# Kernel optimization log

Measured on AMD Instinct MI355X. Metric: run time of the kernel, lower is better.

Reference implementation:

```python
import jax, jax.numpy as jnp
import numpy as np

A, B = 0.0, 1.0
U_LEFT, U_RIGHT = 0.0, 0.0
BOUNDARY_PENALTY = 10.0
N_POINTS = 32768
K_TEST = 1024  # sine test functions
LAYERS = [1, 256, 256, 256, 1]


def setup_inputs() -> dict:
    key = jax.random.key(0)
    ks = jax.random.split(key, 2 + len(LAYERS) - 1)
    # Gauss-Lobatto-like nodes: sorted points in (A, B)
    x = jnp.sort(jax.random.uniform(ks[0], (N_POINTS, 1), dtype=jnp.float32,
                                    minval=A, maxval=B), axis=0)
    # positive quadrature weights, scaled so sum(weights) ~ (B - A)
    weights = jax.random.uniform(ks[1], (N_POINTS,), dtype=jnp.float32) * (2.0 * (B - A) / N_POINTS)
    inp = {"x": x, "weights": weights}
    for i in range(len(LAYERS) - 1):
        fin, fout = LAYERS[i], LAYERS[i + 1]
        inp[f"W{i}"] = jax.random.normal(ks[2 + i], (fin, fout), dtype=jnp.float32) / np.sqrt(fin).astype(np.float32)
        inp[f"b{i}"] = jnp.zeros((fout,), dtype=jnp.float32)
    return inp


def _mlp(h, params):
    # tanh MLP, no activation on the last layer (matches MLP.forward)
    n = len(params)
    for i, (W, b) in enumerate(params):
        h = h @ W + b
        if i < n - 1:
            h = jnp.tanh(h)
    return h


def reference(x, weights, W0, b0, W1, b1, W2, b2, W3, b3):
    params = [(W0, b0), (W1, b1), (W2, b2), (W3, b3)]
    xf = x[:, 0]                                   # [N]

    u = _mlp(x, params)                            # [N, 1]

    # u_xx at every quadrature node via grad-of-grad, vmapped over points
    def u_scalar(xv):
        return _mlp(xv.reshape(1, 1), params)[0, 0]
    u_xx = jax.vmap(jax.grad(jax.grad(u_scalar)))(xf)   # [N]

    # analytic sine test functions v_k(x) = sin(pi k x), k = 1..K
    k = jnp.arange(1, K_TEST + 1, dtype=x.dtype)        # [K]
    test = jnp.sin(jnp.pi * k[:, None] * xf[None, :])   # [K, N]

    source = jnp.sin(jnp.pi * xf)                       # f(x) on the grid, [N]

    # batched quadrature: one matvec replaces the per-k Integrate loop
    Fk = test @ (weights * source)                      # [K]
    Rk = -(test @ (weights * u_xx))                     # [K]  (method 1: -int u_xx v_k)

    loss_interior = jnp.mean((Rk - Fk) ** 2)
    loss_boundary = 0.5 * BOUNDARY_PENALTY * (
        (u[0, 0] - U_LEFT) ** 2 + (u[-1, 0] - U_RIGHT) ** 2
    )
    return jnp.stack([loss_interior, loss_boundary])
```

## Files before the change

### kernel.cpp

```cpp
#include <hip/hip_runtime.h>
#include <cmath>

#define N_PTS 32768
#define HID   256
#define KTEST 1024
#define MB    32
#define RS    264
#define SKC   256
#define SKYB  (N_PTS / SKC)
#define SKGRID (4 * SKYB)
#define NBLK  (N_PTS / MB)

typedef float  f32x4  __attribute__((ext_vector_type(4)));
typedef short  s16x4  __attribute__((ext_vector_type(4)));
typedef short  s16x8  __attribute__((ext_vector_type(8)));
typedef __bf16 bf16x8 __attribute__((ext_vector_type(8)));

__device__ __forceinline__ float b2f(unsigned short s) {
    return __uint_as_float(((unsigned int)s) << 16);
}
__device__ __forceinline__ unsigned short cvt16(float x) {
    return __builtin_bit_cast(unsigned short, (__bf16)x);
}
__device__ __forceinline__ void split2(float x, unsigned short& hi, unsigned short& lo) {
    unsigned int b = __float_as_uint(x);
    hi = (unsigned short)(b >> 16);
    float hf = __uint_as_float(b & 0xFFFF0000u);
    lo = cvt16(x - hf);
}
__device__ __forceinline__ float fast_tanh(float z) {
    float e = __expf(2.0f * z);
    return 1.0f - 2.0f / (e + 1.0f);
}

__global__ __launch_bounds__(64) void wswz_kernel(
    const float* __restrict__ W1, const float* __restrict__ W2,
    unsigned short* __restrict__ Wh1, unsigned short* __restrict__ Wl1,
    unsigned short* __restrict__ Wh2, unsigned short* __restrict__ Wl2,
    unsigned int* __restrict__ counter)
{
    const int lane = threadIdx.x;
    const int t  = blockIdx.x;
    const int kc = blockIdx.y;
    const float* W = blockIdx.z ? W2 : W1;
    unsigned short* Wh = blockIdx.z ? Wh2 : Wh1;
    unsigned short* Wl = blockIdx.z ? Wl2 : Wl1;
    const int q = lane >> 4, ln = lane & 15;
    const int n = t * 16 + ln;
    const int kbase = kc * 32 + q * 8;

    s16x8 hv, lv;
    #pragma unroll
    for (int j = 0; j < 8; ++j) {
        unsigned short h, l;
        split2(W[(kbase + j) * HID + n], h, l);
        hv[j] = (short)h; lv[j] = (short)l;
    }
    const int out = ((t * 8 + kc) * 64 + lane) * 8;
    *(s16x8*)(Wh + out) = hv;
    *(s16x8*)(Wl + out) = lv;

    if (lane == 0 && t == 0 && kc == 0 && blockIdx.z == 0)
        *counter = 0u;
}

__global__ __launch_bounds__(512, 4) void mlp_kernel(
    const float* __restrict__ x, const float* __restrict__ wq,
    const float* __restrict__ W0, const float* __restrict__ b0,
    const float* __restrict__ b1v, const float* __restrict__ b2v,
    const float* __restrict__ W3, const float* __restrict__ b3,
    const unsigned short* __restrict__ W1h, const unsigned short* __restrict__ W1l,
    const unsigned short* __restrict__ W2h, const unsigned short* __restrict__ W2l,
    float* __restrict__ u_arr, float* __restrict__ d_arr,
    float* __restrict__ partF)
{
    __shared__ __align__(16) unsigned short Hb[3][MB][RS];
    __shared__ float sx_h[MB], sx_l[MB], sd[MB];

    const int tid = threadIdx.x;
    const int gp0 = blockIdx.x * MB;

    {
        const int m = tid & 31, seg = tid >> 5;
        const float xm = x[gp0 + m];
        #pragma unroll
        for (int jb = 0; jb < 4; ++jb) {
            s16x4 vy, vyp, vypp;
            #pragma unroll
            for (int jl = 0; jl < 4; ++jl) {
                const int j = seg * 16 + jb * 4 + jl;
                float w = W0[j];
                float z = fmaf(xm, w, b0[j]);
                float y = fast_tanh(z);
                float s = 1.0f - y * y;
                float yp = s * w;
                float ypp = -2.0f * y * yp * w;
                vy[jl]   = (short)cvt16(y);
                vyp[jl]  = (short)cvt16(yp);
                vypp[jl] = (short)cvt16(ypp);
            }
            const int j0 = seg * 16 + jb * 4;
            *(s16x4*)&Hb[0][m][j0] = vy;
            *(s16x4*)&Hb[1][m][j0] = vyp;
            *(s16x4*)&Hb[2][m][j0] = vypp;
        }
    }
    __syncthreads();

    const int lane = tid & 63, wv = tid >> 6;
    const int q = lane >> 4, ln = lane & 15;

    const int fragbase = (wv * 2) * 8 * 512 + lane * 8;

    for (int layer = 0; layer < 2; ++layer) {
        const unsigned short* __restrict__ WhW = (layer ? W2h : W1h) + fragbase;
        const unsigned short* __restrict__ WlW = (layer ? W2l : W1l) + fragbase;
        const float* __restrict__ bb = layer ? b2v : b1v;

        f32x4 acc[3][2][2];
        #pragma unroll
        for (int s = 0; s < 3; ++s)
            #pragma unroll
            for (int mf = 0; mf < 2; ++mf)
                #pragma unroll
                for (int nt = 0; nt < 2; ++nt)
                    acc[s][mf][nt] = (f32x4){0.f, 0.f, 0.f, 0.f};

        s16x8 bh[2][2], bl[2][2];
        #pragma unroll
        for (int nt = 0; nt < 2; ++nt) {
            bh[0][nt] = *(const s16x8*)(WhW + nt * 4096);
            bl[0][nt] = *(const s16x8*)(WlW + nt * 4096);
        }

        int cur = 0;
        for (int kc = 0; kc < 8; ++kc) {
            const int nxt = cur ^ 1;
            if (kc < 7) {
                #pragma unroll
                for (int nt = 0; nt < 2; ++nt) {
                    const int off = nt * 4096 + (kc + 1) * 512;
                    bh[nxt][nt] = *(const s16x8*)(WhW + off);
                    bl[nxt][nt] = *(const s16x8*)(WlW + off);
                }
            }
            s16x8 av[3][2];
            #pragma unroll
            for (int s = 0; s < 3; ++s)
                #pragma unroll
                for (int mf = 0; mf < 2; ++mf)
                    av[s][mf] = *(const s16x8*)&Hb[s][mf * 16 + ln][kc * 32 + q * 8];
            #pragma unroll
            for (int s = 0; s < 3; ++s)
                #pragma unroll
                for (int mf = 0; mf < 2; ++mf)
                    #pragma unroll
                    for (int nt = 0; nt < 2; ++nt) {
                        acc[s][mf][nt] = __builtin_amdgcn_mfma_f32_16x16x32_bf16(
                            __builtin_bit_cast(bf16x8, av[s][mf]),
                            __builtin_bit_cast(bf16x8, bh[cur][nt]), acc[s][mf][nt], 0, 0, 0);
                        acc[s][mf][nt] = __builtin_amdgcn_mfma_f32_16x16x32_bf16(
                            __builtin_bit_cast(bf16x8, av[s][mf]),
                            __builtin_bit_cast(bf16x8, bl[cur][nt]), acc[s][mf][nt], 0, 0, 0);
                    }
            cur = nxt;
        }
        __syncthreads();

        #pragma unroll
        for (int nt = 0; nt < 2; ++nt) {
            const int c = wv * 32 + nt * 16 + ln;
            const float bias = bb[c];
            #pragma unroll
            for (int mf = 0; mf < 2; ++mf) {
                #pragma unroll
                for (int i = 0; i < 4; ++i) {
                    const int r = mf * 16 + q * 4 + i;
                    float z   = acc[0][mf][nt][i] + bias;
                    float zp  = acc[1][mf][nt][i];
                    float zpp = acc[2][mf][nt][i];
                    float y  = fast_tanh(z);
                    float s  = 1.0f - y * y;
                    float yp = s * zp;
                    float ypp = fmaf(s, zpp, -2.0f * y * yp * zp);
                    Hb[0][r][c] = cvt16(y);
                    if (layer == 0) Hb[1][r][c] = cvt16(yp);
                    Hb[2][r][c] = cvt16(ypp);
                }
            }
        }
        __syncthreads();
    }

    float* psum = (float*)&Hb[1][0][0];
    {
        const int m = tid & 31, seg = tid >> 5;
        float su = 0.f, sx = 0.f;
        #pragma unroll
        for (int jj8 = 0; jj8 < 2; ++jj8) {
            const int j0 = seg * 16 + jj8 * 8;
            s16x8 vy = *(const s16x8*)&Hb[0][m][j0];
            s16x8 vx = *(const s16x8*)&Hb[2][m][j0];
            #pragma unroll
            for (int u = 0; u < 8; ++u) {
                float w3 = W3[j0 + u];
                su = fmaf(b2f((unsigned short)vy[u]), w3, su);
                sx = fmaf(b2f((unsigned short)vx[u]), w3, sx);
            }
        }
        psum[(0 * 16 + seg) * 32 + m] = su;
        psum[(1 * 16 + seg) * 32 + m] = sx;
    }
    __syncthreads();
    if (tid < MB) {
        float u = b3[0], uxx = 0.f;
        #pragma unroll
        for (int s2 = 0; s2 < 16; ++s2) {
            u   += psum[s2 * 32 + tid];
            uxx += psum[(16 + s2) * 32 + tid];
        }
        const int gp = gp0 + tid;
        u_arr[gp] = u;
        float xv = x[gp];
        float dv = -wq[gp] * (uxx + sinpif(xv));
        d_arr[gp] = dv;
        float xh = __uint_as_float(__float_as_uint(xv) & 0xFFFFF000u);
        sx_h[tid] = xh * 0.5f;
        sx_l[tid] = (xv - xh) * 0.5f;
        sd[tid]   = dv;
    }

    if (partF) {
        __syncthreads();
        const float k1 = (float)(tid + 1);
        const float k2 = (float)(tid + 513);
        float s1 = 0.f, s2 = 0.f;
        #pragma unroll 8
        for (int i = 0; i < MB; ++i) {
            float xh = sx_h[i], xl = sx_l[i], dv = sd[i];
            float f1 = __builtin_amdgcn_fractf(k1 * xh);
            float t1 = __builtin_amdgcn_fractf(fmaf(k1, xl, f1));
            s1 = fmaf(__builtin_amdgcn_sinf(t1), dv, s1);
            float f2 = __builtin_amdgcn_fractf(k2 * xh);
            float t2 = __builtin_amdgcn_fractf(fmaf(k2, xl, f2));
            s2 = fmaf(__builtin_amdgcn_sinf(t2), dv, s2);
        }
        partF[blockIdx.x * KTEST + tid]       = s1;
        partF[blockIdx.x * KTEST + tid + 512] = s2;
    }
}

__global__ __launch_bounds__(256) void reduce_kernel(
    const float* __restrict__ part, const float* __restrict__ u_arr,
    unsigned int* __restrict__ counter, float* __restrict__ red_g,
    float* __restrict__ out)
{
    __shared__ float sm[8][33];
    __shared__ int lastFlag;

    const int tid = threadIdx.x;
    const int kk = tid & 31;
    const int ch = tid >> 5;
    const int k = blockIdx.x * 32 + kk;

    const float* P = part + (ch << 7) * KTEST + k;
    float s = 0.f;
    #pragma unroll 8
    for (int b = 0; b < 128; ++b) s += P[b << 10];
    sm[ch][kk] = s;
    __syncthreads();

    if (tid < 32) {
        float t = 0.f;
        #pragma unroll
        for (int j = 0; j < 8; ++j) t += sm[j][kk];
        float sq = t * t;
        #pragma unroll
        for (int off = 16; off > 0; off >>= 1) sq += __shfl_down(sq, off, 64);
        if (kk == 0) red_g[blockIdx.x] = sq;
    }
    __threadfence();
    if (tid == 0)
        lastFlag = (atomicAdd(counter, 1u) == 31u);
    __syncthreads();
    if (!lastFlag) return;
    __threadfence();

    if (tid < 32) {
        float v = red_g[tid];
        #pragma unroll
        for (int off = 16; off > 0; off >>= 1) v += __shfl_down(v, off, 64);
        if (tid == 0) {
            out[0] = v * (1.0f / (float)KTEST);
            float u0 = u_arr[0], uN = u_arr[N_PTS - 1];
            out[1] = 5.0f * (u0 * u0 + uN * uN);
        }
    }
}

__global__ __launch_bounds__(256) void sk_loss_kernel(
    const float* __restrict__ x, const float* __restrict__ d_arr,
    const float* __restrict__ u_arr, float* __restrict__ part,
    unsigned int* __restrict__ counter, float* __restrict__ out)
{
    __shared__ float xs_h[SKC], xs_l[SKC], ds[SKC];
    __shared__ float red[4];
    __shared__ int lastFlag;

    const int tid = threadIdx.x;
    const int k = blockIdx.x * 256 + tid;
    const int i0 = blockIdx.y * SKC;

    {
        float xv = x[i0 + tid];
        float xh = __uint_as_float(__float_as_uint(xv) & 0xFFFFF000u);
        xs_h[tid] = xh * 0.5f;
        xs_l[tid] = (xv - xh) * 0.5f;
        ds[tid]   = d_arr[i0 + tid];
    }
    __syncthreads();

    const float kf = (float)(k + 1);
    float s = 0.f;
    #pragma unroll 8
    for (int i = 0; i < SKC; ++i) {
        float A = kf * xs_h[i];
        float f = __builtin_amdgcn_fractf(A);
        float t = __builtin_amdgcn_fractf(fmaf(kf, xs_l[i], f));
        s = fmaf(__builtin_amdgcn_sinf(t), ds[i], s);
    }
    part[blockIdx.y * KTEST + k] = s;

    __threadfence();
    if (tid == 0)
        lastFlag = (atomicAdd(counter, 1u) == (unsigned)(SKGRID - 1));
    __syncthreads();
    if (!lastFlag) return;
    __threadfence();

    float a0 = 0.f, a1 = 0.f, a2 = 0.f, a3 = 0.f;
    const float* P = part + tid * 4;
    for (int yb = 0; yb < SKYB; ++yb) {
        f32x4 v = *(const f32x4*)(P + yb * KTEST);
        a0 += v[0]; a1 += v[1]; a2 += v[2]; a3 += v[3];
    }
    float sq = a0 * a0 + a1 * a1 + a2 * a2 + a3 * a3;
    #pragma unroll
    for (int off = 32; off > 0; off >>= 1) sq += __shfl_down(sq, off, 64);
    if ((tid & 63) == 0) red[tid >> 6] = sq;
    __syncthreads();
    if (tid == 0) {
        float t = red[0] + red[1] + red[2] + red[3];
        out[0] = t * (1.0f / (float)KTEST);
        float u0 = u_arr[0], uN = u_arr[N_PTS - 1];
        out[1] = 5.0f * (u0 * u0 + uN * uN);
    }
}

extern "C" void kernel_launch(void* const* d_in, const int* in_sizes, int n_in,
                              void* d_out, int out_size, void* d_ws, size_t ws_size,
                              hipStream_t stream)
{
    const float* x  = (const float*)d_in[0];
    const float* wq = (const float*)d_in[1];
    const float* W0 = (const float*)d_in[2];
    const float* b0 = (const float*)d_in[3];
    const float* W1 = (const float*)d_in[4];
    const float* b1 = (const float*)d_in[5];
    const float* W2 = (const float*)d_in[6];
    const float* b2 = (const float*)d_in[7];
    const float* W3 = (const float*)d_in[8];
    const float* b3 = (const float*)d_in[9];
    float* out = (float*)d_out;

    float* ws    = (float*)d_ws;
    float* u_arr = ws;
    float* d_arr = ws + N_PTS;
    float* partS = ws + 2 * N_PTS;
    unsigned short* W1h = (unsigned short*)(ws + 2 * N_PTS + SKYB * KTEST);
    unsigned short* W1l = W1h + HID * HID;
    unsigned short* W2h = W1l + HID * HID;
    unsigned short* W2l = W2h + HID * HID;
    unsigned int* counter = (unsigned int*)(W2l + HID * HID);
    float* red_g = ws + 327696;
    float* partF = ws + 327744;
    const size_t need = (size_t)(327744 + NBLK * KTEST) * sizeof(float);
    const bool fused = ws_size >= need;

    wswz_kernel<<<dim3(16, 8, 2), 64, 0, stream>>>(W1, W2, W1h, W1l, W2h, W2l, counter);
    mlp_kernel<<<NBLK, 512, 0, stream>>>(x, wq, W0, b0, b1, b2, W3, b3,
                                         W1h, W1l, W2h, W2l, u_arr, d_arr,
                                         fused ? partF : nullptr);
    if (fused)
        reduce_kernel<<<32, 256, 0, stream>>>(partF, u_arr, counter, red_g, out);
    else
        sk_loss_kernel<<<dim3(4, SKYB), 256, 0, stream>>>(x, d_arr, u_arr, partS, counter, out);
}
```

Before: 131.4 us.

## Fuse sine-projection reduction into MLP kernel via sharded atomics and last-block finish

```diff
diff --git a/kernel.cpp b/kernel.cpp
--- a/kernel.cpp
+++ b/kernel.cpp
@@ -6,10 +6,8 @@
 #define KTEST 1024
 #define MB    32
 #define RS    264
-#define SKC   256
-#define SKYB  (N_PTS / SKC)
-#define SKGRID (4 * SKYB)
 #define NBLK  (N_PTS / MB)
+#define NSHADOW 8
 
 typedef float  f32x4  __attribute__((ext_vector_type(4)));
 typedef short  s16x4  __attribute__((ext_vector_type(4)));
@@ -37,7 +35,7 @@
     const float* __restrict__ W1, const float* __restrict__ W2,
     unsigned short* __restrict__ Wh1, unsigned short* __restrict__ Wl1,
     unsigned short* __restrict__ Wh2, unsigned short* __restrict__ Wl2,
-    unsigned int* __restrict__ counter)
+    unsigned int* __restrict__ counter, float* __restrict__ Rk8)
 {
     const int lane = threadIdx.x;
     const int t  = blockIdx.x;
@@ -60,8 +58,11 @@
     *(s16x8*)(Wh + out) = hv;
     *(s16x8*)(Wl + out) = lv;
 
-    if (lane == 0 && t == 0 && kc == 0 && blockIdx.z == 0)
-        *counter = 0u;
+    if (blockIdx.z == 0) {
+        const int idx = (blockIdx.y * 16 + blockIdx.x) * 64 + lane;
+        Rk8[idx] = 0.f;
+        if (idx == 0) *counter = 0u;
+    }
 }
 
 __global__ __launch_bounds__(512, 4) void mlp_kernel(
@@ -71,11 +72,13 @@
     const float* __restrict__ W3, const float* __restrict__ b3,
     const unsigned short* __restrict__ W1h, const unsigned short* __restrict__ W1l,
     const unsigned short* __restrict__ W2h, const unsigned short* __restrict__ W2l,
-    float* __restrict__ u_arr, float* __restrict__ d_arr,
-    float* __restrict__ partF)
+    float* __restrict__ u_arr, float* __restrict__ Rk8,
+    unsigned int* __restrict__ counter, float* __restrict__ out)
 {
     __shared__ __align__(16) unsigned short Hb[3][MB][RS];
     __shared__ float sx_h[MB], sx_l[MB], sd[MB];
+    __shared__ float red8[8];
+    __shared__ int lastFlag;
 
     const int tid = threadIdx.x;
     const int gp0 = blockIdx.x * MB;
@@ -121,16 +124,16 @@
         #pragma unroll
         for (int s = 0; s < 3; ++s)
             #pragma unroll
-            for (int mf = 0; mf < 2; ++mf)
-                #pragma unroll
-                for (int nt = 0; nt < 2; ++nt)
-                    acc[s][mf][nt] = (f32x4){0.f, 0.f, 0.f, 0.f};
+            for (int mt2 = 0; mt2 < 2; ++mt2)
+                #pragma unroll
+                for (int pt = 0; pt < 2; ++pt)
+                    acc[s][mt2][pt] = (f32x4){0.f, 0.f, 0.f, 0.f};
 
         s16x8 bh[2][2], bl[2][2];
         #pragma unroll
-        for (int nt = 0; nt < 2; ++nt) {
-            bh[0][nt] = *(const s16x8*)(WhW + nt * 4096);
-            bl[0][nt] = *(const s16x8*)(WlW + nt * 4096);
+        for (int mt2 = 0; mt2 < 2; ++mt2) {
+            bh[0][mt2] = *(const s16x8*)(WhW + mt2 * 4096);
+            bl[0][mt2] = *(const s16x8*)(WlW + mt2 * 4096);
         }
 
         int cur = 0;
@@ -138,55 +141,59 @@
             const int nxt = cur ^ 1;
             if (kc < 7) {
                 #pragma unroll
-                for (int nt = 0; nt < 2; ++nt) {
-                    const int off = nt * 4096 + (kc + 1) * 512;
-                    bh[nxt][nt] = *(const s16x8*)(WhW + off);
-                    bl[nxt][nt] = *(const s16x8*)(WlW + off);
+                for (int mt2 = 0; mt2 < 2; ++mt2) {
+                    const int off = mt2 * 4096 + (kc + 1) * 512;
+                    bh[nxt][mt2] = *(const s16x8*)(WhW + off);
+                    bl[nxt][mt2] = *(const s16x8*)(WlW + off);
                 }
             }
             s16x8 av[3][2];
             #pragma unroll
             for (int s = 0; s < 3; ++s)
                 #pragma unroll
-                for (int mf = 0; mf < 2; ++mf)
-                    av[s][mf] = *(const s16x8*)&Hb[s][mf * 16 + ln][kc * 32 + q * 8];
+                for (int pt = 0; pt < 2; ++pt)
+                    av[s][pt] = *(const s16x8*)&Hb[s][pt * 16 + ln][kc * 32 + q * 8];
             #pragma unroll
             for (int s = 0; s < 3; ++s)
                 #pragma unroll
-                for (int mf = 0; mf < 2; ++mf)
+                for (int mt2 = 0; mt2 < 2; ++mt2)
                     #pragma unroll
-                    for (int nt = 0; nt < 2; ++nt) {
-                        acc[s][mf][nt] = __builtin_amdgcn_mfma_f32_16x16x32_bf16(
-                            __builtin_bit_cast(bf16x8, av[s][mf]),
-                            __builtin_bit_cast(bf16x8, bh[cur][nt]), acc[s][mf][nt], 0, 0, 0);
-                        acc[s][mf][nt] = __builtin_amdgcn_mfma_f32_16x16x32_bf16(
-                            __builtin_bit_cast(bf16x8, av[s][mf]),
-                            __builtin_bit_cast(bf16x8, bl[cur][nt]), acc[s][mf][nt], 0, 0, 0);
+                    for (int pt = 0; pt < 2; ++pt) {
+                        acc[s][mt2][pt] = __builtin_amdgcn_mfma_f32_16x16x32_bf16(
+                            __builtin_bit_cast(bf16x8, bh[cur][mt2]),
+                            __builtin_bit_cast(bf16x8, av[s][pt]), acc[s][mt2][pt], 0, 0, 0);
+                        acc[s][mt2][pt] = __builtin_amdgcn_mfma_f32_16x16x32_bf16(
+                            __builtin_bit_cast(bf16x8, bl[cur][mt2]),
+                            __builtin_bit_cast(bf16x8, av[s][pt]), acc[s][mt2][pt], 0, 0, 0);
                     }
             cur = nxt;
         }
         __syncthreads();
 
         #pragma unroll
-        for (int nt = 0; nt < 2; ++nt) {
-            const int c = wv * 32 + nt * 16 + ln;
-            const float bias = bb[c];
-            #pragma unroll
-            for (int mf = 0; mf < 2; ++mf) {
+        for (int pt = 0; pt < 2; ++pt) {
+            const int p = pt * 16 + ln;
+            #pragma unroll
+            for (int mt2 = 0; mt2 < 2; ++mt2) {
+                const int cb = (wv * 2 + mt2) * 16 + q * 4;
+                const f32x4 b4 = *(const f32x4*)&bb[cb];
+                s16x4 vy, vyp, vypp;
                 #pragma unroll
                 for (int i = 0; i < 4; ++i) {
-                    const int r = mf * 16 + q * 4 + i;
-                    float z   = acc[0][mf][nt][i] + bias;
-                    float zp  = acc[1][mf][nt][i];
-                    float zpp = acc[2][mf][nt][i];
+                    float z   = acc[0][mt2][pt][i] + b4[i];
+                    float zp  = acc[1][mt2][pt][i];
+                    float zpp = acc[2][mt2][pt][i];
                     float y  = fast_tanh(z);
                     float s  = 1.0f - y * y;
                     float yp = s * zp;
                     float ypp = fmaf(s, zpp, -2.0f * y * yp * zp);
-                    Hb[0][r][c] = cvt16(y);
-                    if (layer == 0) Hb[1][r][c] = cvt16(yp);
-                    Hb[2][r][c] = cvt16(ypp);
+                    vy[i]   = (short)cvt16(y);
+                    vyp[i]  = (short)cvt16(yp);
+                    vypp[i] = (short)cvt16(ypp);
                 }
+                *(s16x4*)&Hb[0][p][cb] = vy;
+                if (layer == 0) *(s16x4*)&Hb[1][p][cb] = vyp;
+                *(s16x4*)&Hb[2][p][cb] = vypp;
             }
         }
         __syncthreads();
@@ -223,15 +230,14 @@
         u_arr[gp] = u;
         float xv = x[gp];
         float dv = -wq[gp] * (uxx + sinpif(xv));
-        d_arr[gp] = dv;
         float xh = __uint_as_float(__float_as_uint(xv) & 0xFFFFF000u);
         sx_h[tid] = xh * 0.5f;
         sx_l[tid] = (xv - xh) * 0.5f;
         sd[tid]   = dv;
     }
 
-    if (partF) {
-        __syncthreads();
+    __syncthreads();
+    {
         const float k1 = (float)(tid + 1);
         const float k2 = (float)(tid + 513);
         float s1 = 0.f, s2 = 0.f;
@@ -245,113 +251,34 @@
             float t2 = __builtin_amdgcn_fractf(fmaf(k2, xl, f2));
             s2 = fmaf(__builtin_amdgcn_sinf(t2), dv, s2);
         }
-        partF[blockIdx.x * KTEST + tid]       = s1;
-        partF[blockIdx.x * KTEST + tid + 512] = s2;
-    }
-}
-
-__global__ __launch_bounds__(256) void reduce_kernel(
-    const float* __restrict__ part, const float* __restrict__ u_arr,
-    unsigned int* __restrict__ counter, float* __restrict__ red_g,
-    float* __restrict__ out)
-{
-    __shared__ float sm[8][33];
-    __shared__ int lastFlag;
-
-    const int tid = threadIdx.x;
-    const int kk = tid & 31;
-    const int ch = tid >> 5;
-    const int k = blockIdx.x * 32 + kk;
-
-    const float* P = part + (ch << 7) * KTEST + k;
-    float s = 0.f;
-    #pragma unroll 8
-    for (int b = 0; b < 128; ++b) s += P[b << 10];
-    sm[ch][kk] = s;
-    __syncthreads();
-
-    if (tid < 32) {
-        float t = 0.f;
-        #pragma unroll
-        for (int j = 0; j < 8; ++j) t += sm[j][kk];
-        float sq = t * t;
-        #pragma unroll
-        for (int off = 16; off > 0; off >>= 1) sq += __shfl_down(sq, off, 64);
-        if (kk == 0) red_g[blockIdx.x] = sq;
-    }
+        float* myRk = Rk8 + (blockIdx.x & (NSHADOW - 1)) * KTEST;
+        atomicAdd(&myRk[tid], s1);
+        atomicAdd(&myRk[tid + 512], s2);
+    }
+
     __threadfence();
     if (tid == 0)
-        lastFlag = (atomicAdd(counter, 1u) == 31u);
+        lastFlag = (atomicAdd(counter, 1u) == (unsigned)(NBLK - 1));
     __syncthreads();
     if (!lastFlag) return;
     __threadfence();
 
-    if (tid < 32) {
-        float v = red_g[tid];
-        #pragma unroll
-        for (int off = 16; off > 0; off >>= 1) v += __shfl_down(v, off, 64);
-        if (tid == 0) {
-            out[0] = v * (1.0f / (float)KTEST);
-            float u0 = u_arr[0], uN = u_arr[N_PTS - 1];
-            out[1] = 5.0f * (u0 * u0 + uN * uN);
-        }
-    }
-}
-
-__global__ __launch_bounds__(256) void sk_loss_kernel(
-    const float* __restrict__ x, const float* __restrict__ d_arr,
-    const float* __restrict__ u_arr, float* __restrict__ part,
-    unsigned int* __restrict__ counter, float* __restrict__ out)
-{
-    __shared__ float xs_h[SKC], xs_l[SKC], ds[SKC];
-    __shared__ float red[4];
-    __shared__ int lastFlag;
-
-    const int tid = threadIdx.x;
-    const int k = blockIdx.x * 256 + tid;
-    const int i0 = blockIdx.y * SKC;
-
-    {
-        float xv = x[i0 + tid];
-        float xh = __uint_as_float(__float_as_uint(xv) & 0xFFFFF000u);
-        xs_h[tid] = xh * 0.5f;
-        xs_l[tid] = (xv - xh) * 0.5f;
-        ds[tid]   = d_arr[i0 + tid];
-    }
-    __syncthreads();
-
-    const float kf = (float)(k + 1);
-    float s = 0.f;
-    #pragma unroll 8
-    for (int i = 0; i < SKC; ++i) {
-        float A = kf * xs_h[i];
-        float f = __builtin_amdgcn_fractf(A);
-        float t = __builtin_amdgcn_fractf(fmaf(kf, xs_l[i], f));
-        s = fmaf(__builtin_amdgcn_sinf(t), ds[i], s);
-    }
-    part[blockIdx.y * KTEST + k] = s;
-
-    __threadfence();
-    if (tid == 0)
-        lastFlag = (atomicAdd(counter, 1u) == (unsigned)(SKGRID - 1));
-    __syncthreads();
-    if (!lastFlag) return;
-    __threadfence();
-
-    float a0 = 0.f, a1 = 0.f, a2 = 0.f, a3 = 0.f;
-    const float* P = part + tid * 4;
-    for (int yb = 0; yb < SKYB; ++yb) {
-        f32x4 v = *(const f32x4*)(P + yb * KTEST);
-        a0 += v[0]; a1 += v[1]; a2 += v[2]; a3 += v[3];
-    }
-    float sq = a0 * a0 + a1 * a1 + a2 * a2 + a3 * a3;
+    float t0 = 0.f, t1 = 0.f;
+    #pragma unroll
+    for (int j = 0; j < NSHADOW; ++j) {
+        t0 += Rk8[j * KTEST + tid];
+        t1 += Rk8[j * KTEST + tid + 512];
+    }
+    float sq = t0 * t0 + t1 * t1;
     #pragma unroll
     for (int off = 32; off > 0; off >>= 1) sq += __shfl_down(sq, off, 64);
-    if ((tid & 63) == 0) red[tid >> 6] = sq;
+    if ((tid & 63) == 0) red8[tid >> 6] = sq;
     __syncthreads();
     if (tid == 0) {
-        float t = red[0] + red[1] + red[2] + red[3];
-        out[0] = t * (1.0f / (float)KTEST);
+        float tt = 0.f;
+        #pragma unroll
+        for (int j = 0; j < 8; ++j) tt += red8[j];
+        out[0] = tt * (1.0f / (float)KTEST);
         float u0 = u_arr[0], uN = u_arr[N_PTS - 1];
         out[1] = 5.0f * (u0 * u0 + uN * uN);
     }
@@ -375,24 +302,16 @@
 
     float* ws    = (float*)d_ws;
     float* u_arr = ws;
-    float* d_arr = ws + N_PTS;
-    float* partS = ws + 2 * N_PTS;
-    unsigned short* W1h = (unsigned short*)(ws + 2 * N_PTS + SKYB * KTEST);
+    float* Rk8   = ws + N_PTS;
+    unsigned short* W1h = (unsigned short*)(ws + N_PTS + NSHADOW * KTEST);
     unsigned short* W1l = W1h + HID * HID;
     unsigned short* W2h = W1l + HID * HID;
     unsigned short* W2l = W2h + HID * HID;
     unsigned int* counter = (unsigned int*)(W2l + HID * HID);
-    float* red_g = ws + 327696;
-    float* partF = ws + 327744;
-    const size_t need = (size_t)(327744 + NBLK * KTEST) * sizeof(float);
-    const bool fused = ws_size >= need;
-
-    wswz_kernel<<<dim3(16, 8, 2), 64, 0, stream>>>(W1, W2, W1h, W1l, W2h, W2l, counter);
+
+    wswz_kernel<<<dim3(16, 8, 2), 64, 0, stream>>>(W1, W2, W1h, W1l, W2h, W2l,
+                                                   counter, Rk8);
     mlp_kernel<<<NBLK, 512, 0, stream>>>(x, wq, W0, b0, b1, b2, W3, b3,
-                                         W1h, W1l, W2h, W2l, u_arr, d_arr,
-                                         fused ? partF : nullptr);
-    if (fused)
-        reduce_kernel<<<32, 256, 0, stream>>>(partF, u_arr, counter, red_g, out);
-    else
-        sk_loss_kernel<<<dim3(4, SKYB), 256, 0, stream>>>(x, d_arr, u_arr, partS, counter, out);
-}
+                                         W1h, W1l, W2h, W2l, u_arr, Rk8,
+                                         counter, out);
+}
```

Measured after the change: 236.3 us. 79.8% more time.

## Fuse weight conversion, MLP and reduction into one cooperative kernel

Applied to the files above, without the earlier changes.

```diff
diff --git a/kernel.cpp b/kernel.cpp
--- a/kernel.cpp
+++ b/kernel.cpp
@@ -1,15 +1,16 @@
 #include <hip/hip_runtime.h>
+#include <hip/hip_cooperative_groups.h>
 #include <cmath>
+
+namespace cg = cooperative_groups;
 
 #define N_PTS 32768
 #define HID   256
 #define KTEST 1024
 #define MB    32
 #define RS    264
-#define SKC   256
-#define SKYB  (N_PTS / SKC)
-#define SKGRID (4 * SKYB)
 #define NBLK  (N_PTS / MB)
+#define CGRID 512
 
 typedef float  f32x4  __attribute__((ext_vector_type(4)));
 typedef short  s16x4  __attribute__((ext_vector_type(4)));
@@ -33,18 +34,16 @@
     return 1.0f - 2.0f / (e + 1.0f);
 }
 
-__global__ __launch_bounds__(64) void wswz_kernel(
-    const float* __restrict__ W1, const float* __restrict__ W2,
-    unsigned short* __restrict__ Wh1, unsigned short* __restrict__ Wl1,
-    unsigned short* __restrict__ Wh2, unsigned short* __restrict__ Wl2,
-    unsigned int* __restrict__ counter)
-{
-    const int lane = threadIdx.x;
-    const int t  = blockIdx.x;
-    const int kc = blockIdx.y;
-    const float* W = blockIdx.z ? W2 : W1;
-    unsigned short* Wh = blockIdx.z ? Wh2 : Wh1;
-    unsigned short* Wl = blockIdx.z ? Wl2 : Wl1;
+__device__ __forceinline__ void wconv_unit(
+    int vb, int lane,
+    const float* __restrict__ W1r, const float* __restrict__ W2r,
+    unsigned short* __restrict__ W1h, unsigned short* __restrict__ W1l,
+    unsigned short* __restrict__ W2h, unsigned short* __restrict__ W2l)
+{
+    const int t = vb & 15, kc = (vb >> 4) & 7, z = vb >> 7;
+    const float* W = z ? W2r : W1r;
+    unsigned short* Wh = z ? W2h : W1h;
+    unsigned short* Wl = z ? W2l : W1l;
     const int q = lane >> 4, ln = lane & 15;
     const int n = t * 16 + ln;
     const int kbase = kc * 32 + q * 8;
@@ -59,26 +58,21 @@
     const int out = ((t * 8 + kc) * 64 + lane) * 8;
     *(s16x8*)(Wh + out) = hv;
     *(s16x8*)(Wl + out) = lv;
-
-    if (lane == 0 && t == 0 && kc == 0 && blockIdx.z == 0)
-        *counter = 0u;
-}
-
-__global__ __launch_bounds__(512, 4) void mlp_kernel(
+}
+
+__device__ __forceinline__ void mlp_body(
+    const int cb, const int tid,
+    unsigned short (* __restrict__ Hb)[MB][RS],
+    float* __restrict__ sx_h, float* __restrict__ sx_l, float* __restrict__ sd,
     const float* __restrict__ x, const float* __restrict__ wq,
     const float* __restrict__ W0, const float* __restrict__ b0,
     const float* __restrict__ b1v, const float* __restrict__ b2v,
     const float* __restrict__ W3, const float* __restrict__ b3,
     const unsigned short* __restrict__ W1h, const unsigned short* __restrict__ W1l,
     const unsigned short* __restrict__ W2h, const unsigned short* __restrict__ W2l,
-    float* __restrict__ u_arr, float* __restrict__ d_arr,
-    float* __restrict__ partF)
-{
-    __shared__ __align__(16) unsigned short Hb[3][MB][RS];
-    __shared__ float sx_h[MB], sx_l[MB], sd[MB];
-
-    const int tid = threadIdx.x;
-    const int gp0 = blockIdx.x * MB;
+    float* __restrict__ u_arr, float* __restrict__ d_arr, float* __restrict__ partF)
+{
+    const int gp0 = cb * MB;
 
     {
         const int m = tid & 31, seg = tid >> 5;
@@ -230,8 +224,8 @@
         sd[tid]   = dv;
     }
 
-    if (partF) {
-        __syncthreads();
+    __syncthreads();
+    {
         const float k1 = (float)(tid + 1);
         const float k2 = (float)(tid + 513);
         float s1 = 0.f, s2 = 0.f;
@@ -245,9 +239,113 @@
             float t2 = __builtin_amdgcn_fractf(fmaf(k2, xl, f2));
             s2 = fmaf(__builtin_amdgcn_sinf(t2), dv, s2);
         }
-        partF[blockIdx.x * KTEST + tid]       = s1;
-        partF[blockIdx.x * KTEST + tid + 512] = s2;
-    }
+        partF[cb * KTEST + tid]       = s1;
+        partF[cb * KTEST + tid + 512] = s2;
+    }
+}
+
+__global__ __launch_bounds__(512, 4) void fused_kernel(
+    const float* __restrict__ x, const float* __restrict__ wq,
+    const float* __restrict__ W0, const float* __restrict__ b0,
+    const float* __restrict__ W1r, const float* __restrict__ b1v,
+    const float* __restrict__ W2r, const float* __restrict__ b2v,
+    const float* __restrict__ W3, const float* __restrict__ b3,
+    unsigned short* __restrict__ W1h, unsigned short* __restrict__ W1l,
+    unsigned short* __restrict__ W2h, unsigned short* __restrict__ W2l,
+    float* __restrict__ u_arr, float* __restrict__ d_arr,
+    float* __restrict__ partF, unsigned int* __restrict__ counter,
+    float* __restrict__ red_g, float* __restrict__ out)
+{
+    __shared__ __align__(16) unsigned short Hb[3][MB][RS];
+    __shared__ float sx_h[MB], sx_l[MB], sd[MB];
+    __shared__ int lastFlag;
+
+    const int tid = threadIdx.x;
+    const int bx = blockIdx.x;
+    cg::grid_group grid = cg::this_grid();
+
+    if (bx < 256 && tid < 64)
+        wconv_unit(bx, tid, W1r, W2r, W1h, W1l, W2h, W2l);
+    if (bx == 0 && tid == 0) *counter = 0u;
+    __threadfence();
+    grid.sync();
+
+    mlp_body(bx * 2 + 0, tid, Hb, sx_h, sx_l, sd, x, wq, W0, b0, b1v, b2v,
+             W3, b3, W1h, W1l, W2h, W2l, u_arr, d_arr, partF);
+    __syncthreads();
+    mlp_body(bx * 2 + 1, tid, Hb, sx_h, sx_l, sd, x, wq, W0, b0, b1v, b2v,
+             W3, b3, W1h, W1l, W2h, W2l, u_arr, d_arr, partF);
+    __threadfence();
+    grid.sync();
+
+    if (bx >= 32) return;
+    float* smC = (float*)&Hb[0][0][0];
+
+    const int kk = tid & 31;
+    const int ch = tid >> 5;
+    const int k = bx * 32 + kk;
+
+    const float* P = partF + (ch << 6) * KTEST + k;
+    float s = 0.f;
+    #pragma unroll 8
+    for (int b = 0; b < 64; ++b) s += P[b << 10];
+    smC[ch * 33 + kk] = s;
+    __syncthreads();
+
+    if (tid < 32) {
+        float t = 0.f;
+        #pragma unroll
+        for (int j = 0; j < 16; ++j) t += smC[j * 33 + kk];
+        float sq = t * t;
+        #pragma unroll
+        for (int off = 16; off > 0; off >>= 1) sq += __shfl_down(sq, off, 64);
+        if (kk == 0) red_g[bx] = sq;
+    }
+    __threadfence();
+    if (tid == 0)
+        lastFlag = (atomicAdd(counter, 1u) == 31u);
+    __syncthreads();
+    if (!lastFlag) return;
+    __threadfence();
+
+    if (tid < 32) {
+        float v = red_g[tid];
+        #pragma unroll
+        for (int off = 16; off > 0; off >>= 1) v += __shfl_down(v, off, 64);
+        if (tid == 0) {
+            out[0] = v * (1.0f / (float)KTEST);
+            float u0 = u_arr[0], uN = u_arr[N_PTS - 1];
+            out[1] = 5.0f * (u0 * u0 + uN * uN);
+        }
+    }
+}
+
+__global__ __launch_bounds__(64) void wswz_kernel(
+    const float* __restrict__ W1, const float* __restrict__ W2,
+    unsigned short* __restrict__ Wh1, unsigned short* __restrict__ Wl1,
+    unsigned short* __restrict__ Wh2, unsigned short* __restrict__ Wl2,
+    unsigned int* __restrict__ counter)
+{
+    const int vb = (blockIdx.z << 7) | (blockIdx.y << 4) | blockIdx.x;
+    wconv_unit(vb, threadIdx.x,
+               W1, W2, Wh1, Wl1, Wh2, Wl2);
+    if (threadIdx.x == 0 && vb == 0) *counter = 0u;
+}
+
+__global__ __launch_bounds__(512, 4) void mlp_kernel(
+    const float* __restrict__ x, const float* __restrict__ wq,
+    const float* __restrict__ W0, const float* __restrict__ b0,
+    const float* __restrict__ b1v, const float* __restrict__ b2v,
+    const float* __restrict__ W3, const float* __restrict__ b3,
+    const unsigned short* __restrict__ W1h, const unsigned short* __restrict__ W1l,
+    const unsigned short* __restrict__ W2h, const unsigned short* __restrict__ W2l,
+    float* __restrict__ u_arr, float* __restrict__ d_arr,
+    float* __restrict__ partF)
+{
+    __shared__ __align__(16) unsigned short Hb[3][MB][RS];
+    __shared__ float sx_h[MB], sx_l[MB], sd[MB];
+    mlp_body(blockIdx.x, threadIdx.x, Hb, sx_h, sx_l, sd, x, wq, W0, b0,
+             b1v, b2v, W3, b3, W1h, W1l, W2h, W2l, u_arr, d_arr, partF);
 }
 
 __global__ __launch_bounds__(256) void reduce_kernel(
@@ -295,65 +393,6 @@
             float u0 = u_arr[0], uN = u_arr[N_PTS - 1];
             out[1] = 5.0f * (u0 * u0 + uN * uN);
         }
-    }
-}
-
-__global__ __launch_bounds__(256) void sk_loss_kernel(
-    const float* __restrict__ x, const float* __restrict__ d_arr,
-    const float* __restrict__ u_arr, float* __restrict__ part,
-    unsigned int* __restrict__ counter, float* __restrict__ out)
-{
-    __shared__ float xs_h[SKC], xs_l[SKC], ds[SKC];
-    __shared__ float red[4];
-    __shared__ int lastFlag;
-
-    const int tid = threadIdx.x;
-    const int k = blockIdx.x * 256 + tid;
-    const int i0 = blockIdx.y * SKC;
-
-    {
-        float xv = x[i0 + tid];
-        float xh = __uint_as_float(__float_as_uint(xv) & 0xFFFFF000u);
-        xs_h[tid] = xh * 0.5f;
-        xs_l[tid] = (xv - xh) * 0.5f;
-        ds[tid]   = d_arr[i0 + tid];
-    }
-    __syncthreads();
-
-    const float kf = (float)(k + 1);
-    float s = 0.f;
-    #pragma unroll 8
-    for (int i = 0; i < SKC; ++i) {
-        float A = kf * xs_h[i];
-        float f = __builtin_amdgcn_fractf(A);
-        float t = __builtin_amdgcn_fractf(fmaf(kf, xs_l[i], f));
-        s = fmaf(__builtin_amdgcn_sinf(t), ds[i], s);
-    }
-    part[blockIdx.y * KTEST + k] = s;
-
-    __threadfence();
-    if (tid == 0)
-        lastFlag = (atomicAdd(counter, 1u) == (unsigned)(SKGRID - 1));
-    __syncthreads();
-    if (!lastFlag) return;
-    __threadfence();
-
-    float a0 = 0.f, a1 = 0.f, a2 = 0.f, a3 = 0.f;
-    const float* P = part + tid * 4;
-    for (int yb = 0; yb < SKYB; ++yb) {
-        f32x4 v = *(const f32x4*)(P + yb * KTEST);
-        a0 += v[0]; a1 += v[1]; a2 += v[2]; a3 += v[3];
-    }
-    float sq = a0 * a0 + a1 * a1 + a2 * a2 + a3 * a3;
-    #pragma unroll
-    for (int off = 32; off > 0; off >>= 1) sq += __shfl_down(sq, off, 64);
-    if ((tid & 63) == 0) red[tid >> 6] = sq;
-    __syncthreads();
-    if (tid == 0) {
-        float t = red[0] + red[1] + red[2] + red[3];
-        out[0] = t * (1.0f / (float)KTEST);
-        float u0 = u_arr[0], uN = u_arr[N_PTS - 1];
-        out[1] = 5.0f * (u0 * u0 + uN * uN);
     }
 }
 
@@ -376,23 +415,31 @@
     float* ws    = (float*)d_ws;
     float* u_arr = ws;
     float* d_arr = ws + N_PTS;
-    float* partS = ws + 2 * N_PTS;
-    unsigned short* W1h = (unsigned short*)(ws + 2 * N_PTS + SKYB * KTEST);
+    float* partF = ws + 2 * N_PTS;
+    float* red_g = ws + 2 * N_PTS + NBLK * KTEST;
+    unsigned int* counter = (unsigned int*)(red_g + 32);
+    unsigned short* W1h = (unsigned short*)(red_g + 48);
     unsigned short* W1l = W1h + HID * HID;
     unsigned short* W2h = W1l + HID * HID;
     unsigned short* W2l = W2h + HID * HID;
-    unsigned int* counter = (unsigned int*)(W2l + HID * HID);
-    float* red_g = ws + 327696;
-    float* partF = ws + 327744;
-    const size_t need = (size_t)(327744 + NBLK * KTEST) * sizeof(float);
-    const bool fused = ws_size >= need;
-
-    wswz_kernel<<<dim3(16, 8, 2), 64, 0, stream>>>(W1, W2, W1h, W1l, W2h, W2l, counter);
-    mlp_kernel<<<NBLK, 512, 0, stream>>>(x, wq, W0, b0, b1, b2, W3, b3,
-                                         W1h, W1l, W2h, W2l, u_arr, d_arr,
-                                         fused ? partF : nullptr);
-    if (fused)
+
+    void* kargs[] = {
+        (void*)&x, (void*)&wq, (void*)&W0, (void*)&b0, (void*)&W1, (void*)&b1,
+        (void*)&W2, (void*)&b2, (void*)&W3, (void*)&b3,
+        (void*)&W1h, (void*)&W1l, (void*)&W2h, (void*)&W2l,
+        (void*)&u_arr, (void*)&d_arr, (void*)&partF, (void*)&counter,
+        (void*)&red_g, (void*)&out
+    };
+    hipError_t err = hipLaunchCooperativeKernel(
+        (const void*)fused_kernel, dim3(CGRID), dim3(512), kargs, 0, stream);
+
+    if (err != hipSuccess) {
+        (void)hipGetLastError();
+        wswz_kernel<<<dim3(16, 8, 2), 64, 0, stream>>>(W1, W2, W1h, W1l, W2h, W2l,
+                                                       counter);
+        mlp_kernel<<<NBLK, 512, 0, stream>>>(x, wq, W0, b0, b1, b2, W3, b3,
+                                             W1h, W1l, W2h, W2l, u_arr, d_arr,
+                                             partF);
         reduce_kernel<<<32, 256, 0, stream>>>(partF, u_arr, counter, red_g, out);
-    else
-        sk_loss_kernel<<<dim3(4, SKYB), 256, 0, stream>>>(x, d_arr, u_arr, partS, counter, out);
-}
+    }
+}
```

After: 372.3 us. +183.3%, slower.
